# Kernel optimization log

Measured on AMD Instinct MI355X. Metric: run time of the kernel, lower is better.

The kernel has to match this reference:

```python
import jax, jax.numpy as jnp
import numpy as np

N = 4096
FIN = 4096
LOC = 16
H1, H2, HEADS = 120, 50, 4
H1_PER = H1 // HEADS
FILM_Z = 32
SSDB_H = 60
N_HEMI = N // 2
NEG_SLOPE = 0.1
GATE_BIAS = -2.0
MASK_FILL = -9e15


def leaky(x):
    return jax.nn.leaky_relu(x, negative_slope=NEG_SLOPE)


def gat(x, mask, W, a_src, a_dst, bias, concat):
    # x: (N, Fin), W: (H, Fin, O), a_src/a_dst: (H, O), mask: (N, N) bool
    wh = jnp.einsum('nf,hfo->hno', x, W)            # (H, N, O)
    f1 = jnp.einsum('hno,ho->hn', wh, a_src)        # (H, N)
    f2 = jnp.einsum('hno,ho->hn', wh, a_dst)        # (H, N)
    e = leaky(f1[:, :, None] + f2[:, None, :])      # (H, N, N)
    e = jnp.where(mask[None], e, MASK_FILL)
    alpha = jax.nn.softmax(e, axis=-1)
    out = jnp.einsum('hij,hjo->hio', alpha, wh)     # (H, N, O)
    if concat:
        h, n, o = out.shape
        out2 = out.transpose(1, 0, 2).reshape(n, h * o)
    else:
        out2 = out.mean(axis=0)
    return out2 + bias


def _uni(k, shape, stdv):
    return jax.random.uniform(k, shape, jnp.float32, -stdv, stdv)


def setup_inputs() -> dict:
    key = jax.random.key(0)
    ks = jax.random.split(key, 30)
    s1 = 1.0 / np.sqrt(H1_PER)
    s2 = 1.0 / np.sqrt(H2)
    inp = {
        'x_fc': jax.random.normal(ks[0], (N, FIN), jnp.float32),
        'adj': jax.random.randint(ks[1], (N, N), 0, 2, jnp.int32),
        'l_loc': jax.random.uniform(ks[2], (N, LOC), jnp.float32),
        # gat1
        'W1': _uni(ks[3], (HEADS, FIN, H1_PER), s1),
        'a1s': _uni(ks[4], (HEADS, H1_PER), s1),
        'a1d': _uni(ks[5], (HEADS, H1_PER), s1),
        'b1': _uni(ks[6], (H1,), s1),
        # gat2
        'W2': _uni(ks[7], (1, H1, H2), s2),
        'a2s': _uni(ks[8], (1, H2), s2),
        'a2d': _uni(ks[9], (1, H2), s2),
        'b2': _uni(ks[10], (H2,), s2),
        # classifier (no bias)
        'Wc': _uni(ks[11], (2, H2), s2),
        # FiLM trunk
        'Wl1': _uni(ks[12], (FILM_Z, LOC), 1.0 / np.sqrt(LOC)),
        'bl1': _uni(ks[13], (FILM_Z,), 1.0 / np.sqrt(LOC)),
        'Wl2': _uni(ks[14], (FILM_Z, FILM_Z), 1.0 / np.sqrt(FILM_Z)),
        'bl2': _uni(ks[15], (FILM_Z,), 1.0 / np.sqrt(FILM_Z)),
        'Wg': _uni(ks[16], (H2, FILM_Z), 1.0 / np.sqrt(FILM_Z)),
        'bg': _uni(ks[17], (H2,), 1.0 / np.sqrt(FILM_Z)),
        'Wb': _uni(ks[18], (H2, FILM_Z), 1.0 / np.sqrt(FILM_Z)),
        'bb': _uni(ks[19], (H2,), 1.0 / np.sqrt(FILM_Z)),
        'Wgate': _uni(ks[20], (1, FILM_Z), 1.0 / np.sqrt(FILM_Z)),
        'bgate': jnp.full((1,), GATE_BIAS, jnp.float32),
        # SSDB hemi
        'Ws1': _uni(ks[21], (SSDB_H, N_HEMI), 1.0 / np.sqrt(N_HEMI)),
        'bs1': _uni(ks[22], (SSDB_H,), 1.0 / np.sqrt(N_HEMI)),
        'Ws2': _uni(ks[23], (1, SSDB_H), 1.0 / np.sqrt(SSDB_H)),
        'bs2': _uni(ks[24], (1,), 1.0 / np.sqrt(SSDB_H)),
    }
    return inp


def reference(x_fc, adj, l_loc, W1, a1s, a1d, b1, W2, a2s, a2d, b2, Wc,
              Wl1, bl1, Wl2, bl2, Wg, bg, Wb, bb, Wgate, bgate,
              Ws1, bs1, Ws2, bs2):
    mask = adj > 0
    h = leaky(gat(x_fc, mask, W1, a1s, a1d, b1, concat=True))    # (N, 120)
    h = leaky(gat(h, mask, W2, a2s, a2d, b2, concat=False))      # (N, 50)
    # FiLM conditioning
    z = leaky(l_loc @ Wl1.T + bl1)
    z = leaky(z @ Wl2.T + bl2)
    gamma = z @ Wg.T + bg                                        # (N, 50)
    beta = z @ Wb.T + bb                                         # (N, 50)
    g = jax.nn.sigmoid(z @ Wgate.T + bgate)                      # (N, 1)
    cov = jnp.clip(l_loc[:, -1], 0.0, 1.0)                       # coverage_power = 1.0
    g = g * cov[:, None]
    h_fused = h + g * (gamma * h + beta)
    logits = leaky(h_fused @ Wc.T)                               # (N, 2)
    # hemisphere SSDB bias
    t = logits.T                                                 # (2, N)
    ipsi = t[:, :N_HEMI]
    contra = t[:, N_HEMI:2 * N_HEMI]
    h_i = leaky(ipsi @ Ws1.T + bs1)                              # (2, 60)
    h_c = leaky(contra @ Ws1.T + bs1)
    b_i = leaky(h_i @ Ws2.T + bs2)                               # (2, 1)
    b_c = leaky(h_c @ Ws2.T + bs2)
    b_mid = 0.5 * (b_i + b_c)                                    # (2, 1)
    bias_nodes = jnp.concatenate([
        jnp.broadcast_to(b_i.T, (N_HEMI, 2)),
        jnp.broadcast_to(b_c.T, (N_HEMI, 2)),
    ], axis=0)                                                   # n_mid = 0
    logits = logits + bias_nodes
    bias_avg = b_mid[:, 0]                                       # (2,)
    return logits, bias_avg
```

## Files before the change

### kernel.cpp

```cpp
#include <hip/hip_runtime.h>

#define NN 4096
#define HEADS 4
#define H1PER 30
#define H1DIM 120
#define H2DIM 50

typedef short short8_t __attribute__((ext_vector_type(8)));
typedef float f32x4 __attribute__((ext_vector_type(4)));

__device__ __forceinline__ float lrelu(float x) { return x > 0.f ? x : 0.1f * x; }

__device__ __forceinline__ unsigned short bfrne(float x) {
  unsigned u = __float_as_uint(x);
  u += 0x7fffu + ((u >> 16) & 1u);
  return (unsigned short)(u >> 16);
}
__device__ __forceinline__ unsigned bfpk_rne(float lo, float hi) {
  return (unsigned)bfrne(lo) | ((unsigned)bfrne(hi) << 16);
}
__device__ __forceinline__ unsigned bfpk(float lo, float hi) {
  unsigned a = (__float_as_uint(lo) + 0x8000u) >> 16;
  unsigned b = (__float_as_uint(hi) + 0x8000u) & 0xffff0000u;
  return a | b;
}
__device__ __forceinline__ float score(float f2v, float f1r, float mr, unsigned bsel, int jj) {
  float f = f1r + f2v;
  float e = fmaxf(f, 0.1f * f);
  float wv = __expf(e - mr);
  return wv * (float)((bsel >> jj) & 1u);
}

#define GL16(g, l)                                                                        \
  __builtin_amdgcn_global_load_lds((const __attribute__((address_space(1))) unsigned int*)(g), \
                                   (__attribute__((address_space(3))) unsigned int*)(l), 16, 0, 0)

__global__ __launch_bounds__(256) void k_bits(const int* __restrict__ adj,
                                              unsigned long long* __restrict__ bits) {
  size_t base = (size_t)blockIdx.x * 1024;
  int t = threadIdx.x;
  int v0 = adj[base + t];
  int v1 = adj[base + 256 + t];
  int v2 = adj[base + 512 + t];
  int v3 = adj[base + 768 + t];
  unsigned long long m0 = __ballot(v0 > 0);
  unsigned long long m1 = __ballot(v1 > 0);
  unsigned long long m2 = __ballot(v2 > 0);
  unsigned long long m3 = __ballot(v3 > 0);
  if ((t & 63) == 0) {
    size_t w = (base + t) >> 6;
    bits[w] = m0;
    bits[w + 4] = m1;
    bits[w + 8] = m2;
    bits[w + 12] = m3;
  }
}

__global__ __launch_bounds__(256) void k_prep(const float* __restrict__ W1,
                                              const float* __restrict__ a1s,
                                              const float* __restrict__ a1d,
                                              unsigned short* __restrict__ w1t) {
  int k = blockIdx.x * 256 + threadIdx.x;
#pragma unroll
  for (int h = 0; h < 4; ++h) {
    const float* wp = W1 + ((size_t)h * 4096 + k) * H1PER;
    float fs = 0.f, fd = 0.f;
#pragma unroll
    for (int oo = 0; oo < H1PER; ++oo) {
      float v = wp[oo];
      w1t[(size_t)(h * 30 + oo) * 4096 + k] = bfrne(v);
      fs += v * a1s[h * H1PER + oo];
      fd += v * a1d[h * H1PER + oo];
    }
    w1t[(size_t)(120 + h) * 4096 + k] = bfrne(fs);
    w1t[(size_t)(124 + h) * 4096 + k] = bfrne(fd);
  }
}

__global__ __launch_bounds__(256) void k_gemm1s(const float* __restrict__ x,
                                                const unsigned short* __restrict__ w1t,
                                                float* __restrict__ part) {
  const int t = threadIdx.x;
  const int lane = t & 63, wave = t >> 6;
  const int m = lane & 15, q = lane >> 4;
  const int i0 = blockIdx.x * 32;
  const int kz = blockIdx.y * 512;
  __shared__ float xs[32 * 64];
  const int r0 = (wave & 1) * 16;
  const int ntg0 = (wave >> 1) * 4;
  const int srow0 = wave * 8 + q;
  const int srow1 = srow0 + 4;
  const int sc0 = m ^ (srow0 & 7);
  const int sc1 = m ^ (srow1 & 7);
  const float* gx0 = x + (size_t)(i0 + srow0) * 4096 + kz + sc0 * 4;
  const float* gx1 = x + (size_t)(i0 + srow1) * 4096 + kz + sc1 * 4;
  float* ls0 = &xs[srow0 * 64 + m * 4];
  float* ls1 = &xs[srow1 * 64 + m * 4];
  const int arow = r0 + m;
  const int asw = (m & 7);
  f32x4 acc[4];
#pragma unroll
  for (int nt = 0; nt < 4; ++nt) acc[nt] = (f32x4){0.f, 0.f, 0.f, 0.f};
  for (int it = 0; it < 8; ++it) {
    const int kc = it * 64;
    GL16(gx0 + kc, ls0);
    GL16(gx1 + kc, ls1);
    __syncthreads();
#pragma unroll
    for (int ks2 = 0; ks2 < 2; ++ks2) {
      const int c0 = ks2 * 8 + q * 2;
      float4 a0 = *(const float4*)&xs[arow * 64 + ((c0 ^ asw) * 4)];
      float4 a1 = *(const float4*)&xs[arow * 64 + (((c0 + 1) ^ asw) * 4)];
      union { short8_t v; unsigned u[4]; } A;
      A.u[0] = bfpk_rne(a0.x, a0.y);
      A.u[1] = bfpk_rne(a0.z, a0.w);
      A.u[2] = bfpk_rne(a1.x, a1.y);
      A.u[3] = bfpk_rne(a1.z, a1.w);
      const unsigned short* wp = w1t + (size_t)m * 4096 + kz + kc + ks2 * 32 + q * 8;
#pragma unroll
      for (int nt = 0; nt < 4; ++nt) {
        short8_t B = *(const short8_t*)(wp + (size_t)(ntg0 + nt) * 16 * 4096);
        acc[nt] = __builtin_amdgcn_mfma_f32_16x16x32_bf16(A.v, B, acc[nt], 0, 0, 0);
      }
    }
    __syncthreads();
  }
  float* pp = part + ((size_t)blockIdx.y * 4096 + i0 + r0 + q * 4) * 128 + ntg0 * 16 + m;
#pragma unroll
  for (int nt = 0; nt < 4; ++nt)
#pragma unroll
    for (int r = 0; r < 4; ++r) pp[r * 128 + nt * 16] = acc[nt][r];
}

__global__ __launch_bounds__(256) void k_f1c(const float* __restrict__ part,
                                             unsigned short* __restrict__ whbt,
                                             float* __restrict__ f1, float* __restrict__ f2) {
  const int t = threadIdx.x;
  const int n = blockIdx.x * 16 + (t >> 4);
  const int og = (t & 15) * 8;
  float s[8] = {0.f, 0.f, 0.f, 0.f, 0.f, 0.f, 0.f, 0.f};
  for (int z = 0; z < 8; ++z) {
    const float* pp = part + ((size_t)z * NN + n) * 128 + og;
    float4 u0 = *(const float4*)pp;
    float4 u1 = *(const float4*)(pp + 4);
    s[0] += u0.x; s[1] += u0.y; s[2] += u0.z; s[3] += u0.w;
    s[4] += u1.x; s[5] += u1.y; s[6] += u1.z; s[7] += u1.w;
  }
  if (og < 120) {
#pragma unroll
    for (int j = 0; j < 8; ++j) {
      int o = og + j;
      int h = o / 30, oo = o - h * 30;
      whbt[(size_t)(h * 32 + oo) * NN + n] = bfrne(s[j]);
    }
  } else {
#pragma unroll
    for (int j = 0; j < 4; ++j) {
      f1[(size_t)j * NN + n] = s[j];
      f2[(size_t)j * NN + n] = s[4 + j];
    }
  }
  if ((t & 15) < 8) {
    int h = (t & 15) >> 1, odd = (t & 15) & 1;
    whbt[(size_t)(h * 32 + 30 + odd) * NN + n] = odd ? 0 : 0x3f80;
  }
}

__global__ __launch_bounds__(256) void k_max(const float* __restrict__ v, float* __restrict__ mx) {
  int t = threadIdx.x;
  const float* row = v + (size_t)blockIdx.x * NN;
  float m = -3.0e38f;
  for (int n = t; n < NN; n += 256) m = fmaxf(m, row[n]);
  for (int off = 32; off > 0; off >>= 1) m = fmaxf(m, __shfl_down(m, off));
  __shared__ float ms[4];
  if ((t & 63) == 0) ms[t >> 6] = m;
  __syncthreads();
  if (t == 0) mx[blockIdx.x] = fmaxf(fmaxf(ms[0], ms[1]), fmaxf(ms[2], ms[3]));
}

__global__ __launch_bounds__(256) void k_att1m(const unsigned short* __restrict__ whbt,
                                               const float* __restrict__ f1, const float* __restrict__ f2,
                                               const float* __restrict__ mx,
                                               const unsigned int* __restrict__ bits32,
                                               float* __restrict__ part) {
  const int h = blockIdx.y, js = blockIdx.z;
  const int t = threadIdx.x;
  const int lane = t & 63, wave = t >> 6;
  const int m = lane & 15, q = lane >> 4;
  const int i0 = blockIdx.x * 64 + wave * 16;
  const int jbase = js * 2048;
  __shared__ float f2s[2048];
  for (int e = t; e < 2048; e += 256) f2s[e] = f2[h * NN + jbase + e];
  __syncthreads();
  const float f1r = f1[h * NN + i0 + m];
  const float fm = f1r + mx[h];
  const float mr = fmaxf(fm, 0.1f * fm);
  const unsigned int* brow = bits32 + (size_t)(i0 + m) * 128 + (jbase >> 5);
  const unsigned short* bb0 = whbt + (size_t)(h * 32 + m) * NN + jbase + q * 8;
  const unsigned short* bb1 = bb0 + 16 * NN;
  const float* fp = f2s + q * 8;
  f32x4 acc0 = {0.f, 0.f, 0.f, 0.f}, acc1 = {0.f, 0.f, 0.f, 0.f};
  for (int step = 0; step < 64; ++step) {
    const int jl = step * 32;
    unsigned bsel = brow[step] >> (q * 8);
    float4 fa = *(const float4*)(fp + jl);
    float4 fb = *(const float4*)(fp + jl + 4);
    float w0 = score(fa.x, f1r, mr, bsel, 0);
    float w1 = score(fa.y, f1r, mr, bsel, 1);
    float w2 = score(fa.z, f1r, mr, bsel, 2);
    float w3 = score(fa.w, f1r, mr, bsel, 3);
    float w4 = score(fb.x, f1r, mr, bsel, 4);
    float w5 = score(fb.y, f1r, mr, bsel, 5);
    float w6 = score(fb.z, f1r, mr, bsel, 6);
    float w7 = score(fb.w, f1r, mr, bsel, 7);
    union { short8_t v; unsigned u[4]; } A;
    A.u[0] = bfpk(w0, w1);
    A.u[1] = bfpk(w2, w3);
    A.u[2] = bfpk(w4, w5);
    A.u[3] = bfpk(w6, w7);
    short8_t b0 = *(const short8_t*)(bb0 + jl);
    short8_t b1 = *(const short8_t*)(bb1 + jl);
    acc0 = __builtin_amdgcn_mfma_f32_16x16x32_bf16(A.v, b0, acc0, 0, 0, 0);
    acc1 = __builtin_amdgcn_mfma_f32_16x16x32_bf16(A.v, b1, acc1, 0, 0, 0);
  }
  float* pp = part + ((size_t)(js * 4 + h) * NN + i0 + q * 4) * 32 + m;
#pragma unroll
  for (int r = 0; r < 4; ++r) {
    pp[r * 32] = acc0[r];
    pp[r * 32 + 16] = acc1[r];
  }
}

__global__ __launch_bounds__(256) void k_h1(const float* __restrict__ part, const float* __restrict__ b1,
                                            float* __restrict__ h1) {
  int t = threadIdx.x;
  int lane = t & 63;
  int p = lane >> 5, o = lane & 31;
  int id = blockIdx.x * 8 + (t >> 6) * 2 + p;
  int h = id >> 12, n = id & 4095;
  const float* p0 = part + ((size_t)h * NN + n) * 32 + o;
  const float* p1 = part + ((size_t)(4 + h) * NN + n) * 32 + o;
  float tot = p0[0] + p1[0];
  float l = __shfl(tot, p * 32 + 30);
  if (o < H1PER) h1[(size_t)n * H1DIM + h * H1PER + o] = lrelu(tot / l + b1[h * H1PER + o]);
}

__global__ __launch_bounds__(256) void k_gemm2(const float* __restrict__ h1, const float* __restrict__ W2,
                                               float* __restrict__ wh2) {
  const int n0 = blockIdx.x * 4;
  const int t = threadIdx.x;
  const int o = t & 63, r = t >> 6;
  __shared__ float hs[4][120];
  for (int e = t; e < 4 * H1DIM; e += 256) hs[e / H1DIM][e % H1DIM] = h1[(size_t)n0 * H1DIM + e];
  __syncthreads();
  if (o < H2DIM) {
    float acc = 0.f;
#pragma unroll 4
    for (int k = 0; k < H1DIM; ++k) acc += hs[r][k] * W2[k * H2DIM + o];
    wh2[(size_t)(n0 + r) * H2DIM + o] = acc;
  }
}

__global__ __launch_bounds__(256) void k_f2l2(const float* __restrict__ wh2, const float* __restrict__ a2s,
                                              const float* __restrict__ a2d, float* __restrict__ f1,
                                              float* __restrict__ f2, unsigned short* __restrict__ whbt) {
  int n = blockIdx.x * 256 + threadIdx.x;
  if (n >= NN) return;
  const float* r = wh2 + (size_t)n * H2DIM;
  unsigned short* wb = whbt + n;
  float accs = 0.f, accd = 0.f;
#pragma unroll
  for (int j = 0; j < H2DIM; ++j) {
    float v = r[j];
    wb[j * NN] = bfrne(v);
    accs += v * a2s[j];
    accd += v * a2d[j];
  }
  wb[50 * NN] = 0x3f80;
#pragma unroll
  for (int j = 51; j < 64; ++j) wb[j * NN] = 0;
  f1[n] = accs;
  f2[n] = accd;
}

__global__ __launch_bounds__(256) void k_att2m(const unsigned short* __restrict__ whbt,
                                               const float* __restrict__ f1, const float* __restrict__ f2,
                                               const float* __restrict__ mx,
                                               const unsigned int* __restrict__ bits32,
                                               float* __restrict__ part) {
  const int js = blockIdx.y;
  const int t = threadIdx.x;
  const int lane = t & 63, wave = t >> 6;
  const int m = lane & 15, q = lane >> 4;
  const int i0 = blockIdx.x * 64 + wave * 16;
  const int jbase = js * 1024;
  __shared__ float f2s[1024];
  for (int e = t; e < 1024; e += 256) f2s[e] = f2[jbase + e];
  __syncthreads();
  const float f1r = f1[i0 + m];
  const float fm = f1r + mx[0];
  const float mr = fmaxf(fm, 0.1f * fm);
  const unsigned int* brow = bits32 + (size_t)(i0 + m) * 128 + (jbase >> 5);
  const unsigned short* bb = whbt + (size_t)m * NN + jbase + q * 8;
  const float* fp = f2s + q * 8;
  f32x4 acc[4];
#pragma unroll
  for (int x = 0; x < 4; ++x) acc[x] = (f32x4){0.f, 0.f, 0.f, 0.f};
  for (int step = 0; step < 32; ++step) {
    const int jl = step * 32;
    unsigned bsel = brow[step] >> (q * 8);
    float4 fa = *(const float4*)(fp + jl);
    float4 fb = *(const float4*)(fp + jl + 4);
    float w0 = score(fa.x, f1r, mr, bsel, 0);
    float w1 = score(fa.y, f1r, mr, bsel, 1);
    float w2 = score(fa.z, f1r, mr, bsel, 2);
    float w3 = score(fa.w, f1r, mr, bsel, 3);
    float w4 = score(fb.x, f1r, mr, bsel, 4);
    float w5 = score(fb.y, f1r, mr, bsel, 5);
    float w6 = score(fb.z, f1r, mr, bsel, 6);
    float w7 = score(fb.w, f1r, mr, bsel, 7);
    union { short8_t v; unsigned u[4]; } A;
    A.u[0] = bfpk(w0, w1);
    A.u[1] = bfpk(w2, w3);
    A.u[2] = bfpk(w4, w5);
    A.u[3] = bfpk(w6, w7);
#pragma unroll
    for (int tile = 0; tile < 4; ++tile) {
      short8_t b = *(const short8_t*)(bb + (size_t)tile * 16 * NN + jl);
      acc[tile] = __builtin_amdgcn_mfma_f32_16x16x32_bf16(A.v, b, acc[tile], 0, 0, 0);
    }
  }
  float* pp = part + ((size_t)js * NN + i0 + q * 4) * 64 + m;
#pragma unroll
  for (int tile = 0; tile < 4; ++tile)
#pragma unroll
    for (int r = 0; r < 4; ++r) pp[r * 64 + tile * 16] = acc[tile][r];
}

__global__ __launch_bounds__(64) void k_h2(const float* __restrict__ part, const float* __restrict__ b2,
                                           float* __restrict__ h2) {
  int n = blockIdx.x;
  int o = threadIdx.x;
  const float* p = part + (size_t)n * 64 + o;
  float tot = p[0] + p[NN * 64] + p[2 * NN * 64] + p[3 * NN * 64];
  float l = __shfl(tot, 50);
  if (o < H2DIM) h2[(size_t)n * H2DIM + o] = lrelu(tot / l + b2[o]);
}

__global__ __launch_bounds__(256) void k_film(const float* __restrict__ l_loc, const float* __restrict__ h2,
                                              const float* __restrict__ Wl1, const float* __restrict__ bl1,
                                              const float* __restrict__ Wl2, const float* __restrict__ bl2,
                                              const float* __restrict__ Wg, const float* __restrict__ bg,
                                              const float* __restrict__ Wb, const float* __restrict__ bb,
                                              const float* __restrict__ Wgate, const float* __restrict__ bgate,
                                              const float* __restrict__ Wc, float* __restrict__ logits) {
  int n = blockIdx.x * 4 + (threadIdx.x >> 6);
  int lane = threadIdx.x & 63;
  int r32 = lane & 31;
  float locv = l_loc[n * 16 + (lane & 15)];
  float cov = __shfl(locv, 15);
  cov = fminf(fmaxf(cov, 0.f), 1.f);
  float a1v = bl1[r32];
#pragma unroll
  for (int j = 0; j < 16; ++j) a1v += Wl1[r32 * 16 + j] * __shfl(locv, j);
  float z1 = lrelu(a1v);
  float a2v = bl2[r32];
#pragma unroll
  for (int j = 0; j < 32; ++j) a2v += Wl2[r32 * 32 + j] * __shfl(z1, j);
  float z2 = lrelu(a2v);
  float gs = bgate[0];
  float gam, bet;
  {
    int o = lane < H2DIM ? lane : 0;
    gam = bg[o];
    bet = bb[o];
#pragma unroll
    for (int j = 0; j < 32; ++j) {
      float zj = __shfl(z2, j);
      gs += Wgate[j] * zj;
      gam += Wg[o * 32 + j] * zj;
      bet += Wb[o * 32 + j] * zj;
    }
  }
  float g = cov / (1.f + __expf(-gs));
  int o = lane < H2DIM ? lane : 0;
  float hv = h2[(size_t)n * H2DIM + o];
  float hf = hv + g * (gam * hv + bet);
  float p0 = lane < H2DIM ? hf * Wc[o] : 0.f;
  float p1 = lane < H2DIM ? hf * Wc[H2DIM + o] : 0.f;
  for (int off = 32; off > 0; off >>= 1) {
    p0 += __shfl_down(p0, off);
    p1 += __shfl_down(p1, off);
  }
  if (lane == 0) {
    logits[n * 2 + 0] = lrelu(p0);
    logits[n * 2 + 1] = lrelu(p1);
  }
}

__global__ __launch_bounds__(64) void k_ssdb1(const float* __restrict__ logits, const float* __restrict__ Ws1,
                                              float* __restrict__ hsum) {
  int combo = blockIdx.y;
  int hemi = combo >> 1, c = combo & 1;
  int k = threadIdx.x;
  if (k >= 60) return;
  int nbase = blockIdx.x * 256;
  const float* wrow = Ws1 + (size_t)k * 2048 + nbase;
  const float* lcol = logits + (size_t)(hemi * 2048 + nbase) * 2 + c;
  float part = 0.f;
  for (int q = 0; q < 256; ++q) part += wrow[q] * lcol[2 * q];
  atomicAdd(&hsum[combo * 60 + k], part);
}

__global__ __launch_bounds__(256) void k_ssdb2(const float* __restrict__ hsum, const float* __restrict__ bs1,
                                               const float* __restrict__ Ws2, const float* __restrict__ bs2,
                                               float* __restrict__ B) {
  int t = threadIdx.x;
  int combo = t >> 6, k = t & 63;
  float part = 0.f;
  if (k < 60) part = lrelu(hsum[combo * 60 + k] + bs1[k]) * Ws2[k];
  for (int off = 32; off > 0; off >>= 1) part += __shfl_down(part, off);
  if (k == 0) B[combo] = lrelu(part + bs2[0]);
}

__global__ __launch_bounds__(256) void k_final(const float* __restrict__ logits, const float* __restrict__ B,
                                               float* __restrict__ out) {
  int id = blockIdx.x * 256 + threadIdx.x;
  if (id < 2 * NN) {
    int n = id >> 1, c = id & 1;
    out[id] = logits[id] + B[(n < 2048 ? 0 : 2) + c];
  } else if (id < 2 * NN + 2) {
    int c = id - 2 * NN;
    out[id] = 0.5f * (B[c] + B[2 + c]);
  }
}

#define OFF_BITS 0
#define OFF_W1T 524288
#define OFF_GP 786432
#define OFF_A1P 786432
#define OFF_A2P 1835008
#define OFF_H1 2883584
#define OFF_WH2 3375104
#define OFF_WH2BT 3579904
#define OFF_F12 3710976
#define OFF_F22 3715072
#define OFF_MX2 3719168
#define OFF_H2 3719232
#define OFF_LOG 3924032
#define OFF_HSUM 3932224
#define OFF_B 3932480
#define OFF_WH1BT 9175040
#define OFF_F1A 9437184
#define OFF_F2A 9453568
#define OFF_MX1 9469952

extern "C" void kernel_launch(void* const* d_in, const int* in_sizes, int n_in,
                              void* d_out, int out_size, void* d_ws, size_t ws_size,
                              hipStream_t stream) {
  const float* x_fc  = (const float*)d_in[0];
  const int*   adj   = (const int*)d_in[1];
  const float* l_loc = (const float*)d_in[2];
  const float* W1    = (const float*)d_in[3];
  const float* a1s   = (const float*)d_in[4];
  const float* a1d   = (const float*)d_in[5];
  const float* b1    = (const float*)d_in[6];
  const float* W2    = (const float*)d_in[7];
  const float* a2s   = (const float*)d_in[8];
  const float* a2d   = (const float*)d_in[9];
  const float* b2    = (const float*)d_in[10];
  const float* Wc    = (const float*)d_in[11];
  const float* Wl1   = (const float*)d_in[12];
  const float* bl1   = (const float*)d_in[13];
  const float* Wl2   = (const float*)d_in[14];
  const float* bl2   = (const float*)d_in[15];
  const float* Wg    = (const float*)d_in[16];
  const float* bg    = (const float*)d_in[17];
  const float* Wb    = (const float*)d_in[18];
  const float* bb    = (const float*)d_in[19];
  const float* Wgate = (const float*)d_in[20];
  const float* bgate = (const float*)d_in[21];
  const float* Ws1   = (const float*)d_in[22];
  const float* bs1   = (const float*)d_in[23];
  const float* Ws2   = (const float*)d_in[24];
  const float* bs2   = (const float*)d_in[25];
  float* out = (float*)d_out;
  float* w = (float*)d_ws;
  unsigned long long* bits = (unsigned long long*)(w + OFF_BITS);
  const unsigned int* bits32 = (const unsigned int*)bits;
  unsigned short* wh1bt = (unsigned short*)(w + OFF_WH1BT);
  unsigned short* wh2bt = (unsigned short*)(w + OFF_WH2BT);
  unsigned short* w1t = (unsigned short*)(w + OFF_W1T);

  k_bits<<<NN * NN / 1024, 256, 0, stream>>>(adj, bits);
  k_prep<<<16, 256, 0, stream>>>(W1, a1s, a1d, w1t);
  k_gemm1s<<<dim3(128, 8), 256, 0, stream>>>(x_fc, w1t, w + OFF_GP);
  k_f1c<<<256, 256, 0, stream>>>(w + OFF_GP, wh1bt, w + OFF_F1A, w + OFF_F2A);
  k_max<<<HEADS, 256, 0, stream>>>(w + OFF_F2A, w + OFF_MX1);
  k_att1m<<<dim3(64, HEADS, 2), 256, 0, stream>>>(wh1bt, w + OFF_F1A, w + OFF_F2A,
                                                  w + OFF_MX1, bits32, w + OFF_A1P);
  k_h1<<<2048, 256, 0, stream>>>(w + OFF_A1P, b1, w + OFF_H1);
  k_gemm2<<<NN / 4, 256, 0, stream>>>(w + OFF_H1, W2, w + OFF_WH2);
  k_f2l2<<<NN / 256, 256, 0, stream>>>(w + OFF_WH2, a2s, a2d, w + OFF_F12, w + OFF_F22, wh2bt);
  k_max<<<1, 256, 0, stream>>>(w + OFF_F22, w + OFF_MX2);
  k_att2m<<<dim3(64, 4), 256, 0, stream>>>(wh2bt, w + OFF_F12, w + OFF_F22,
                                           w + OFF_MX2, bits32, w + OFF_A2P);
  k_h2<<<NN, 64, 0, stream>>>(w + OFF_A2P, b2, w + OFF_H2);
  k_film<<<NN / 4, 256, 0, stream>>>(l_loc, w + OFF_H2, Wl1, bl1, Wl2, bl2, Wg, bg, Wb, bb,
                                     Wgate, bgate, Wc, w + OFF_LOG);
  hipMemsetAsync(w + OFF_HSUM, 0, 240 * sizeof(float), stream);
  k_ssdb1<<<dim3(8, 4), 64, 0, stream>>>(w + OFF_LOG, Ws1, w + OFF_HSUM);
  k_ssdb2<<<1, 256, 0, stream>>>(w + OFF_HSUM, bs1, Ws2, bs2, w + OFF_B);
  k_final<<<(2 * NN + 2 + 255) / 256, 256, 0, stream>>>(w + OFF_LOG, w + OFF_B, out);
}
```

Before: 359.2 us.

## Factor attention exp into per-row and per-column terms; double j-split

The attention score exp(leaky(f1+f2)-m) is split into precomputed per-column exponentials (for the positive and the negative-slope branches) times per-row constants. A threshold compare picks the branch, so the per-element __expf disappears from the MFMA loop. Both attention kernels also split the j dimension into twice as many blocks for more parallelism, and the reduction kernels sum the extra partials. k_h2 now handles four nodes per block, and the att2 partial buffer reuses the att1 region. The cost is more partial-sum traffic and a changed rounding path, including possible overflow or underflow in the factored exponentials.

```diff
diff --git a/kernel.cpp b/kernel.cpp
--- a/kernel.cpp
+++ b/kernel.cpp
@@ -23,12 +23,6 @@
   unsigned a = (__float_as_uint(lo) + 0x8000u) >> 16;
   unsigned b = (__float_as_uint(hi) + 0x8000u) & 0xffff0000u;
   return a | b;
-}
-__device__ __forceinline__ float score(float f2v, float f1r, float mr, unsigned bsel, int jj) {
-  float f = f1r + f2v;
-  float e = fmaxf(f, 0.1f * f);
-  float wv = __expf(e - mr);
-  return wv * (float)((bsel >> jj) & 1u);
 }
 
 #define GL16(g, l)                                                                        \
@@ -188,31 +182,43 @@
   const int lane = t & 63, wave = t >> 6;
   const int m = lane & 15, q = lane >> 4;
   const int i0 = blockIdx.x * 64 + wave * 16;
-  const int jbase = js * 2048;
-  __shared__ float f2s[2048];
-  for (int e = t; e < 2048; e += 256) f2s[e] = f2[h * NN + jbase + e];
+  const int jbase = js * 1024;
+  const float mxh = mx[h];
+  __shared__ float2 es[1024];
+  for (int e = t; e < 1024; e += 256) {
+    float fv = f2[h * NN + jbase + e] - mxh;
+    es[e] = make_float2(__expf(fv), __expf(0.1f * fv));
+  }
   __syncthreads();
   const float f1r = f1[h * NN + i0 + m];
-  const float fm = f1r + mx[h];
-  const float mr = fmaxf(fm, 0.1f * fm);
+  const float s = f1r + mxh;
+  const float C1 = __expf(fminf(0.f, 0.9f * s));
+  const float C2 = __expf(fminf(0.f, -0.9f * s));
+  const float Tr = __expf(-s);
   const unsigned int* brow = bits32 + (size_t)(i0 + m) * 128 + (jbase >> 5);
   const unsigned short* bb0 = whbt + (size_t)(h * 32 + m) * NN + jbase + q * 8;
   const unsigned short* bb1 = bb0 + 16 * NN;
-  const float* fp = f2s + q * 8;
+  const float2* fp = es + q * 8;
   f32x4 acc0 = {0.f, 0.f, 0.f, 0.f}, acc1 = {0.f, 0.f, 0.f, 0.f};
-  for (int step = 0; step < 64; ++step) {
+  for (int step = 0; step < 32; ++step) {
     const int jl = step * 32;
     unsigned bsel = brow[step] >> (q * 8);
-    float4 fa = *(const float4*)(fp + jl);
-    float4 fb = *(const float4*)(fp + jl + 4);
-    float w0 = score(fa.x, f1r, mr, bsel, 0);
-    float w1 = score(fa.y, f1r, mr, bsel, 1);
-    float w2 = score(fa.z, f1r, mr, bsel, 2);
-    float w3 = score(fa.w, f1r, mr, bsel, 3);
-    float w4 = score(fb.x, f1r, mr, bsel, 4);
-    float w5 = score(fb.y, f1r, mr, bsel, 5);
-    float w6 = score(fb.z, f1r, mr, bsel, 6);
-    float w7 = score(fb.w, f1r, mr, bsel, 7);
+    float4 e01 = *(const float4*)(fp + jl);
+    float4 e23 = *(const float4*)(fp + jl + 2);
+    float4 e45 = *(const float4*)(fp + jl + 4);
+    float4 e67 = *(const float4*)(fp + jl + 6);
+    auto sc = [&](float ep, float en, int jj) {
+      float wv = (ep > Tr) ? C1 * ep : C2 * en;
+      return ((bsel >> jj) & 1u) ? wv : 0.f;
+    };
+    float w0 = sc(e01.x, e01.y, 0);
+    float w1 = sc(e01.z, e01.w, 1);
+    float w2 = sc(e23.x, e23.y, 2);
+    float w3 = sc(e23.z, e23.w, 3);
+    float w4 = sc(e45.x, e45.y, 4);
+    float w5 = sc(e45.z, e45.w, 5);
+    float w6 = sc(e67.x, e67.y, 6);
+    float w7 = sc(e67.z, e67.w, 7);
     union { short8_t v; unsigned u[4]; } A;
     A.u[0] = bfpk(w0, w1);
     A.u[1] = bfpk(w2, w3);
@@ -238,9 +244,9 @@
   int p = lane >> 5, o = lane & 31;
   int id = blockIdx.x * 8 + (t >> 6) * 2 + p;
   int h = id >> 12, n = id & 4095;
-  const float* p0 = part + ((size_t)h * NN + n) * 32 + o;
-  const float* p1 = part + ((size_t)(4 + h) * NN + n) * 32 + o;
-  float tot = p0[0] + p1[0];
+  float tot = 0.f;
+#pragma unroll
+  for (int z = 0; z < 4; ++z) tot += part[((size_t)(z * 4 + h) * NN + n) * 32 + o];
   float l = __shfl(tot, p * 32 + 30);
   if (o < H1PER) h1[(size_t)n * H1DIM + h * H1PER + o] = lrelu(tot / l + b1[h * H1PER + o]);
 }
@@ -293,32 +299,44 @@
   const int lane = t & 63, wave = t >> 6;
   const int m = lane & 15, q = lane >> 4;
   const int i0 = blockIdx.x * 64 + wave * 16;
-  const int jbase = js * 1024;
-  __shared__ float f2s[1024];
-  for (int e = t; e < 1024; e += 256) f2s[e] = f2[jbase + e];
+  const int jbase = js * 512;
+  const float mx0 = mx[0];
+  __shared__ float2 es[512];
+  for (int e = t; e < 512; e += 256) {
+    float fv = f2[jbase + e] - mx0;
+    es[e] = make_float2(__expf(fv), __expf(0.1f * fv));
+  }
   __syncthreads();
   const float f1r = f1[i0 + m];
-  const float fm = f1r + mx[0];
-  const float mr = fmaxf(fm, 0.1f * fm);
+  const float s = f1r + mx0;
+  const float C1 = __expf(fminf(0.f, 0.9f * s));
+  const float C2 = __expf(fminf(0.f, -0.9f * s));
+  const float Tr = __expf(-s);
   const unsigned int* brow = bits32 + (size_t)(i0 + m) * 128 + (jbase >> 5);
   const unsigned short* bb = whbt + (size_t)m * NN + jbase + q * 8;
-  const float* fp = f2s + q * 8;
+  const float2* fp = es + q * 8;
   f32x4 acc[4];
 #pragma unroll
   for (int x = 0; x < 4; ++x) acc[x] = (f32x4){0.f, 0.f, 0.f, 0.f};
-  for (int step = 0; step < 32; ++step) {
+  for (int step = 0; step < 16; ++step) {
     const int jl = step * 32;
     unsigned bsel = brow[step] >> (q * 8);
-    float4 fa = *(const float4*)(fp + jl);
-    float4 fb = *(const float4*)(fp + jl + 4);
-    float w0 = score(fa.x, f1r, mr, bsel, 0);
-    float w1 = score(fa.y, f1r, mr, bsel, 1);
-    float w2 = score(fa.z, f1r, mr, bsel, 2);
-    float w3 = score(fa.w, f1r, mr, bsel, 3);
-    float w4 = score(fb.x, f1r, mr, bsel, 4);
-    float w5 = score(fb.y, f1r, mr, bsel, 5);
-    float w6 = score(fb.z, f1r, mr, bsel, 6);
-    float w7 = score(fb.w, f1r, mr, bsel, 7);
+    float4 e01 = *(const float4*)(fp + jl);
+    float4 e23 = *(const float4*)(fp + jl + 2);
+    float4 e45 = *(const float4*)(fp + jl + 4);
+    float4 e67 = *(const float4*)(fp + jl + 6);
+    auto sc = [&](float ep, float en, int jj) {
+      float wv = (ep > Tr) ? C1 * ep : C2 * en;
+      return ((bsel >> jj) & 1u) ? wv : 0.f;
+    };
+    float w0 = sc(e01.x, e01.y, 0);
+    float w1 = sc(e01.z, e01.w, 1);
+    float w2 = sc(e23.x, e23.y, 2);
+    float w3 = sc(e23.z, e23.w, 3);
+    float w4 = sc(e45.x, e45.y, 4);
+    float w5 = sc(e45.z, e45.w, 5);
+    float w6 = sc(e67.x, e67.y, 6);
+    float w7 = sc(e67.z, e67.w, 7);
     union { short8_t v; unsigned u[4]; } A;
     A.u[0] = bfpk(w0, w1);
     A.u[1] = bfpk(w2, w3);
@@ -337,12 +355,15 @@
     for (int r = 0; r < 4; ++r) pp[r * 64 + tile * 16] = acc[tile][r];
 }
 
-__global__ __launch_bounds__(64) void k_h2(const float* __restrict__ part, const float* __restrict__ b2,
-                                           float* __restrict__ h2) {
-  int n = blockIdx.x;
-  int o = threadIdx.x;
+__global__ __launch_bounds__(256) void k_h2(const float* __restrict__ part, const float* __restrict__ b2,
+                                            float* __restrict__ h2) {
+  int t = threadIdx.x;
+  int n = blockIdx.x * 4 + (t >> 6);
+  int o = t & 63;
   const float* p = part + (size_t)n * 64 + o;
-  float tot = p[0] + p[NN * 64] + p[2 * NN * 64] + p[3 * NN * 64];
+  float tot = 0.f;
+#pragma unroll
+  for (int z = 0; z < 8; ++z) tot += p[(size_t)z * NN * 64];
   float l = __shfl(tot, 50);
   if (o < H2DIM) h2[(size_t)n * H2DIM + o] = lrelu(tot / l + b2[o]);
 }
@@ -439,7 +460,7 @@
 #define OFF_W1T 524288
 #define OFF_GP 786432
 #define OFF_A1P 786432
-#define OFF_A2P 1835008
+#define OFF_A2P 786432
 #define OFF_H1 2883584
 #define OFF_WH2 3375104
 #define OFF_WH2BT 3579904
@@ -497,15 +518,15 @@
   k_gemm1s<<<dim3(128, 8), 256, 0, stream>>>(x_fc, w1t, w + OFF_GP);
   k_f1c<<<256, 256, 0, stream>>>(w + OFF_GP, wh1bt, w + OFF_F1A, w + OFF_F2A);
   k_max<<<HEADS, 256, 0, stream>>>(w + OFF_F2A, w + OFF_MX1);
-  k_att1m<<<dim3(64, HEADS, 2), 256, 0, stream>>>(wh1bt, w + OFF_F1A, w + OFF_F2A,
+  k_att1m<<<dim3(64, HEADS, 4), 256, 0, stream>>>(wh1bt, w + OFF_F1A, w + OFF_F2A,
                                                   w + OFF_MX1, bits32, w + OFF_A1P);
   k_h1<<<2048, 256, 0, stream>>>(w + OFF_A1P, b1, w + OFF_H1);
   k_gemm2<<<NN / 4, 256, 0, stream>>>(w + OFF_H1, W2, w + OFF_WH2);
   k_f2l2<<<NN / 256, 256, 0, stream>>>(w + OFF_WH2, a2s, a2d, w + OFF_F12, w + OFF_F22, wh2bt);
   k_max<<<1, 256, 0, stream>>>(w + OFF_F22, w + OFF_MX2);
-  k_att2m<<<dim3(64, 4), 256, 0, stream>>>(wh2bt, w + OFF_F12, w + OFF_F22,
+  k_att2m<<<dim3(64, 8), 256, 0, stream>>>(wh2bt, w + OFF_F12, w + OFF_F22,
                                            w + OFF_MX2, bits32, w + OFF_A2P);
-  k_h2<<<NN, 64, 0, stream>>>(w + OFF_A2P, b2, w + OFF_H2);
+  k_h2<<<NN / 4, 256, 0, stream>>>(w + OFF_A2P, b2, w + OFF_H2);
   k_film<<<NN / 4, 256, 0, stream>>>(l_loc, w + OFF_H2, Wl1, bl1, Wl2, bl2, Wg, bg, Wb, bb,
                                      Wgate, bgate, Wc, w + OFF_LOG);
   hipMemsetAsync(w + OFF_HSUM, 0, 240 * sizeof(float), stream);
```

Measured after the change: 366.8 us. +2.1%, slower.
